# Optimization experiments

Hardware: AMD Instinct MI355X
Metric: run time of the kernel (lower is better)

Reference implementation:

```python
import jax, jax.numpy as jnp
import numpy as np

HEADS = 8
EMB = 128

def setup_inputs() -> dict:
    key = jax.random.key(0)
    ks = jax.random.split(key, 5)
    b, t, hin = 4, 128, 1024
    N = 50000
    x = jax.random.normal(ks[0], (b, t, hin), dtype=jnp.float32)
    curiosity_score = jax.random.normal(ks[1], (b, t), dtype=jnp.float32)
    Wq = jax.random.normal(ks[2], (EMB * HEADS, hin), dtype=jnp.float32) * (1.0 / np.sqrt(hin))
    keys = jax.random.normal(ks[3], (N, EMB), dtype=jnp.float32)
    values = jax.random.normal(ks[4], (N,), dtype=jnp.float32)
    return {"x": x, "curiosity_score": curiosity_score, "Wq": Wq, "keys": keys, "values": values}

def reference(x, curiosity_score, Wq, keys, values):
    b, t, hin = x.shape
    h, e = HEADS, EMB
    # query projection (torch Linear, no bias): x @ Wq.T -> (b, t, h*e)
    q = jnp.einsum('bti,oi->bto', x, Wq).reshape(b, t, h, e)
    q = q / (e ** 0.25)
    # scores vs shared offline key bank (N, e); buffer was `heads` identical copies,
    # so broadcasting over h is the same math without materializing repeats.
    scores = jnp.einsum('bthe,ne->bthn', q, keys)          # (b, t, h, N)
    attn = jax.nn.softmax(scores, axis=-1)
    # weighted sum of scalar values; curiosity adds a per-query constant to every
    # value, and since attn rows sum to 1 this equals adding curiosity afterwards.
    out = jnp.einsum('bthn,n->bth', attn, values) + curiosity_score[:, :, None]
    out = out.mean(axis=2)                                  # mean over heads
    return out[:, :, None]                                  # (b, t, 1)
```

## Files before the change

kernel.cpp:

```cpp
#include <hip/hip_runtime.h>

#define NHEADS   8
#define EMB_     128
#define BT_      512
#define HIN_     1024
#define NQ_      4096
#define NKEY_    50000
#define NPAD_    50048
#define TILES_TOT 782
#define TPS_     17
#define NSLICES_ 46

#define QSCALE   (0.29730177875068026f * 1.4426950408889634f)

typedef __attribute__((ext_vector_type(8))) short short8v;
typedef __attribute__((ext_vector_type(4))) float float4v;

#if __has_builtin(__builtin_amdgcn_exp2f)
#define EXP2F(x) __builtin_amdgcn_exp2f(x)
#else
#define EXP2F(x) exp2f(x)
#endif

__device__ __forceinline__ short f2bf(float f) {
  unsigned u = __float_as_uint(f);
  u += 0x7fffu + ((u >> 16) & 1u);
  return (short)(u >> 16);
}

#if __has_builtin(__builtin_amdgcn_cvt_pk_bf16_f32)
typedef __attribute__((ext_vector_type(2))) __bf16 bf16x2;
__device__ __forceinline__ unsigned pk2(float a, float b) {
  bf16x2 r = __builtin_amdgcn_cvt_pk_bf16_f32(a, b);
  union { bf16x2 v; unsigned u; } c; c.v = r; return c.u;
}
#else
__device__ __forceinline__ unsigned pk2(float a, float b) {
  return (unsigned)(unsigned short)f2bf(a) | ((unsigned)(unsigned short)f2bf(b) << 16);
}
#endif

__global__ __launch_bounds__(256) void convert_kernel(
    const float* __restrict__ keys, const float* __restrict__ values,
    short* __restrict__ keys_sw, float* __restrict__ vpad) {
#pragma unroll
  for (int j = 0; j < 2; ++j) {
    int g = blockIdx.x * 512 + j * 256 + threadIdx.x;
    int key  = g >> 5;
    int posf = g & 31;
    int lc   = posf >> 1;
    int half = posf & 1;
    union { short4 s; unsigned u[2]; } o;
    if (key < NKEY_) {
      float4 v = ((const float4*)keys)[g];
      o.u[0] = pk2(v.x, v.y);
      o.u[1] = pk2(v.z, v.w);
    } else {
      o.u[0] = 0; o.u[1] = 0;
    }
    int pc = lc ^ (key & 15);
    *(short4*)(keys_sw + key * 128 + pc * 8 + half * 4) = o.s;
    if (posf == 0) vpad[key] = (key < NKEY_) ? values[key] : 0.f;
  }
}

__global__ __launch_bounds__(256) void proj_kernel(
    const float* __restrict__ x, const float* __restrict__ Wq,
    short* __restrict__ qb) {
  const int wave = threadIdx.x >> 6, lane = threadIdx.x & 63;
  const int quad = lane >> 4, ln = lane & 15;
  const int tile = blockIdx.x * 4 + wave;
  const int mt = tile >> 6, ot = tile & 63;
  const float* xrow = x  + (mt * 16 + ln) * HIN_ + quad * 8;
  const float* wrow = Wq + (ot * 16 + ln) * HIN_ + quad * 8;
  float4v d = {0.f, 0.f, 0.f, 0.f};

  float4 xa0 = *(const float4*)(xrow);
  float4 xa1 = *(const float4*)(xrow + 4);
  float4 wa0 = *(const float4*)(wrow);
  float4 wa1 = *(const float4*)(wrow + 4);
  float4 xb0 = *(const float4*)(xrow + 32);
  float4 xb1 = *(const float4*)(xrow + 36);
  float4 wb0 = *(const float4*)(wrow + 32);
  float4 wb1 = *(const float4*)(wrow + 36);

#pragma unroll 1
  for (int k0 = 0; k0 < HIN_; k0 += 64) {
    union { short8v s8; unsigned u[4]; } af, bf;
    af.u[0] = pk2(xa0.x, xa0.y); af.u[1] = pk2(xa0.z, xa0.w);
    af.u[2] = pk2(xa1.x, xa1.y); af.u[3] = pk2(xa1.z, xa1.w);
    bf.u[0] = pk2(wa0.x, wa0.y); bf.u[1] = pk2(wa0.z, wa0.w);
    bf.u[2] = pk2(wa1.x, wa1.y); bf.u[3] = pk2(wa1.z, wa1.w);
    if (k0 + 64 < HIN_) {
      xa0 = *(const float4*)(xrow + k0 + 64);
      xa1 = *(const float4*)(xrow + k0 + 68);
      wa0 = *(const float4*)(wrow + k0 + 64);
      wa1 = *(const float4*)(wrow + k0 + 68);
    }
    d = __builtin_amdgcn_mfma_f32_16x16x32_bf16(af.s8, bf.s8, d, 0, 0, 0);

    af.u[0] = pk2(xb0.x, xb0.y); af.u[1] = pk2(xb0.z, xb0.w);
    af.u[2] = pk2(xb1.x, xb1.y); af.u[3] = pk2(xb1.z, xb1.w);
    bf.u[0] = pk2(wb0.x, wb0.y); bf.u[1] = pk2(wb0.z, wb0.w);
    bf.u[2] = pk2(wb1.x, wb1.y); bf.u[3] = pk2(wb1.z, wb1.w);
    if (k0 + 96 < HIN_) {
      xb0 = *(const float4*)(xrow + k0 + 96);
      xb1 = *(const float4*)(xrow + k0 + 100);
      wb0 = *(const float4*)(wrow + k0 + 96);
      wb1 = *(const float4*)(wrow + k0 + 100);
    }
    d = __builtin_amdgcn_mfma_f32_16x16x32_bf16(af.s8, bf.s8, d, 0, 0, 0);
  }
#pragma unroll
  for (int r2 = 0; r2 < 4; ++r2)
    qb[(mt * 16 + quad * 4 + r2) * HIN_ + ot * 16 + ln] = f2bf(d[r2] * QSCALE);
}

__global__ __launch_bounds__(256) void attn_kernel(
    const short* __restrict__ qb,
    const short* __restrict__ keys_sw,
    const float* __restrict__ vpad,
    float* __restrict__ partials) {
  __shared__ __align__(16) short kt[2][64 * 128];
  const int t     = threadIdx.x;
  const int wave  = t >> 6;
  const int lane  = t & 63;
  const int quad  = lane >> 4;
  const int ln    = lane & 15;
  const int qbase = blockIdx.x * 256 + wave * 64;
  const int slice = blockIdx.y;
  const int tile0 = slice * TPS_;
  const int tile1 = tile0 + TPS_;

  short8v a[4][4];
#pragma unroll
  for (int sub = 0; sub < 4; ++sub)
#pragma unroll
    for (int ks = 0; ks < 4; ++ks)
      a[sub][ks] = *(const short8v*)(qb + (qbase + sub * 16 + ln) * EMB_ + ks * 32 + quad * 8);

  float lsum[4][4], asum[4][4];
#pragma unroll
  for (int i = 0; i < 4; ++i)
#pragma unroll
    for (int j = 0; j < 4; ++j) { lsum[i][j] = 0.f; asum[i][j] = 0.f; }

  short8v stage[4];
  float vcur, vnext;
  {
    const short* src = keys_sw + tile0 * (64 * 128);
#pragma unroll
    for (int j = 0; j < 4; ++j)
      stage[j] = *(const short8v*)(src + (t + j * 256) * 8);
    vcur = vpad[tile0 * 64 + lane];
#pragma unroll
    for (int j = 0; j < 4; ++j)
      *(short8v*)(&kt[0][0] + (t + j * 256) * 8) = stage[j];
    const short* s1 = keys_sw + (tile0 + 1) * (64 * 128);
#pragma unroll
    for (int j = 0; j < 4; ++j)
      stage[j] = *(const short8v*)(s1 + (t + j * 256) * 8);
    vnext = vpad[(tile0 + 1) * 64 + lane];
  }
  __syncthreads();

  for (int tile = tile0; tile < tile1; ++tile) {
    const int cur = (tile - tile0) & 1;
    if (tile + 1 < tile1) {
#pragma unroll
      for (int j = 0; j < 4; ++j)
        *(short8v*)(&kt[cur ^ 1][0] + (t + j * 256) * 8) = stage[j];
    }
    const float vt = vcur;
    vcur = vnext;
    if (tile + 2 < tile1) {
      const short* nsrc = keys_sw + (tile + 2) * (64 * 128);
#pragma unroll
      for (int j = 0; j < 4; ++j)
        stage[j] = *(const short8v*)(nsrc + (t + j * 256) * 8);
      vnext = vpad[(tile + 2) * 64 + lane];
    }
#pragma unroll
    for (int nsub = 0; nsub < 4; ++nsub) {
      short8v b[4];
#pragma unroll
      for (int ks = 0; ks < 4; ++ks) {
        int kc = ks * 4 + quad;
        b[ks] = *(const short8v*)(&kt[cur][0] + (nsub * 16 + ln) * EMB_ + ((kc ^ ln) * 8));
      }
      float v = __shfl(vt, nsub * 16 + ln, 64);
      float4v d[4];
#pragma unroll
      for (int sub = 0; sub < 4; ++sub) d[sub] = (float4v){0.f, 0.f, 0.f, 0.f};
#pragma unroll
      for (int ks = 0; ks < 4; ++ks)
#pragma unroll
        for (int sub = 0; sub < 4; ++sub)
          d[sub] = __builtin_amdgcn_mfma_f32_16x16x32_bf16(a[sub][ks], b[ks], d[sub], 0, 0, 0);
#pragma unroll
      for (int sub = 0; sub < 4; ++sub)
#pragma unroll
        for (int r2 = 0; r2 < 4; ++r2) {
          float p = EXP2F(d[sub][r2]);
          lsum[sub][r2] += p;
          asum[sub][r2] = fmaf(p, v, asum[sub][r2]);
        }
    }
    __syncthreads();
  }

#pragma unroll
  for (int sub = 0; sub < 4; ++sub)
#pragma unroll
    for (int r2 = 0; r2 < 4; ++r2) {
      float L = lsum[sub][r2], A = asum[sub][r2];
#pragma unroll
      for (int m = 1; m < 16; m <<= 1) {
        L += __shfl_xor(L, m, 64);
        A += __shfl_xor(A, m, 64);
      }
      if (ln == 0) {
        int q = qbase + sub * 16 + quad * 4 + r2;
        partials[(q * NSLICES_ + slice) * 2 + 0] = L;
        partials[(q * NSLICES_ + slice) * 2 + 1] = A;
      }
    }
}

__global__ __launch_bounds__(256) void finalize_kernel(
    const float* __restrict__ partials, const float* __restrict__ cur,
    float* __restrict__ out) {
  int tid = blockIdx.x * 256 + threadIdx.x;
  int bt = tid >> 3, h = tid & 7;
  int q = bt * NHEADS + h;
  const float4* p = (const float4*)(partials + q * NSLICES_ * 2);
  float sl = 0.f, sa = 0.f;
#pragma unroll
  for (int i = 0; i < NSLICES_ / 2; ++i) {
    float4 v = p[i];
    sl += v.x + v.z;
    sa += v.y + v.w;
  }
  float r = sa / sl;
  r += __shfl_xor(r, 1, 64);
  r += __shfl_xor(r, 2, 64);
  r += __shfl_xor(r, 4, 64);
  if (h == 0) out[bt] = r * (1.f / NHEADS) + cur[bt];
}

extern "C" void kernel_launch(void* const* d_in, const int* in_sizes, int n_in,
                              void* d_out, int out_size, void* d_ws, size_t ws_size,
                              hipStream_t stream) {
  (void)in_sizes; (void)n_in; (void)out_size; (void)ws_size;
  const float* x      = (const float*)d_in[0];
  const float* cur    = (const float*)d_in[1];
  const float* Wq     = (const float*)d_in[2];
  const float* keys   = (const float*)d_in[3];
  const float* values = (const float*)d_in[4];
  float* out = (float*)d_out;

  char* ws = (char*)d_ws;
  short* keys_sw = (short*)(ws);
  float* vpad    = (float*)(ws + 12812288);
  short* qb      = (short*)(ws + 13012480);
  float* part    = (float*)(ws + 14061056);

  hipLaunchKernelGGL(convert_kernel, dim3((NPAD_ * 32) / 512), dim3(256), 0, stream,
                     keys, values, keys_sw, vpad);
  hipLaunchKernelGGL(proj_kernel, dim3(512), dim3(256), 0, stream, x, Wq, qb);
  hipLaunchKernelGGL(attn_kernel, dim3(16, NSLICES_), dim3(256), 0, stream,
                     qb, keys_sw, vpad, part);
  hipLaunchKernelGGL(finalize_kernel, dim3(16), dim3(256), 0, stream, part, cur, out);
}
```

Measured before the change: 176.3 us.

## Store keys in MFMA fragment order and load B operands directly from global

The convert kernel now writes the bf16 keys in the exact per-lane MFMA B-fragment order, in groups of 16 keys. The attention kernel then drops the shared-memory double buffer and its block barriers. Each wave loads its B fragments straight from global memory (L2/L1) with a two-group register prefetch. This removes LDS traffic and __syncthreads. The cost is that each of the four waves loads the same key data redundantly from cache, and the loads have less latency hiding than the block-staged tiles did.

```diff
diff --git a/kernel.cpp b/kernel.cpp
--- a/kernel.cpp
+++ b/kernel.cpp
@@ -7,8 +7,8 @@
 #define NQ_      4096
 #define NKEY_    50000
 #define NPAD_    50048
-#define TILES_TOT 782
-#define TPS_     17
+#define NGRP_    3128
+#define GPS_     68
 #define NSLICES_ 46
 
 #define QSCALE   (0.29730177875068026f * 1.4426950408889634f)
@@ -42,7 +42,7 @@
 
 __global__ __launch_bounds__(256) void convert_kernel(
     const float* __restrict__ keys, const float* __restrict__ values,
-    short* __restrict__ keys_sw, float* __restrict__ vpad) {
+    short* __restrict__ keys_fr, float* __restrict__ vpad) {
 #pragma unroll
   for (int j = 0; j < 2; ++j) {
     int g = blockIdx.x * 512 + j * 256 + threadIdx.x;
@@ -58,8 +58,9 @@
     } else {
       o.u[0] = 0; o.u[1] = 0;
     }
-    int pc = lc ^ (key & 15);
-    *(short4*)(keys_sw + key * 128 + pc * 8 + half * 4) = o.s;
+    int grp = key >> 4, kln = key & 15;
+    int ks = lc >> 2, q = lc & 3;
+    *(short4*)(keys_fr + ((grp * 4 + ks) * 64 + q * 16 + kln) * 8 + half * 4) = o.s;
     if (posf == 0) vpad[key] = (key < NKEY_) ? values[key] : 0.f;
   }
 }
@@ -118,10 +119,9 @@
 
 __global__ __launch_bounds__(256) void attn_kernel(
     const short* __restrict__ qb,
-    const short* __restrict__ keys_sw,
+    const short* __restrict__ keys_fr,
     const float* __restrict__ vpad,
     float* __restrict__ partials) {
-  __shared__ __align__(16) short kt[2][64 * 128];
   const int t     = threadIdx.x;
   const int wave  = t >> 6;
   const int lane  = t & 63;
@@ -129,8 +129,8 @@
   const int ln    = lane & 15;
   const int qbase = blockIdx.x * 256 + wave * 64;
   const int slice = blockIdx.y;
-  const int tile0 = slice * TPS_;
-  const int tile1 = tile0 + TPS_;
+  const int g0    = slice * GPS_;
+  const int g1    = g0 + GPS_;
 
   short8v a[4][4];
 #pragma unroll
@@ -145,50 +145,20 @@
 #pragma unroll
     for (int j = 0; j < 4; ++j) { lsum[i][j] = 0.f; asum[i][j] = 0.f; }
 
-  short8v stage[4];
-  float vcur, vnext;
-  {
-    const short* src = keys_sw + tile0 * (64 * 128);
-#pragma unroll
-    for (int j = 0; j < 4; ++j)
-      stage[j] = *(const short8v*)(src + (t + j * 256) * 8);
-    vcur = vpad[tile0 * 64 + lane];
-#pragma unroll
-    for (int j = 0; j < 4; ++j)
-      *(short8v*)(&kt[0][0] + (t + j * 256) * 8) = stage[j];
-    const short* s1 = keys_sw + (tile0 + 1) * (64 * 128);
-#pragma unroll
-    for (int j = 0; j < 4; ++j)
-      stage[j] = *(const short8v*)(s1 + (t + j * 256) * 8);
-    vnext = vpad[(tile0 + 1) * 64 + lane];
-  }
-  __syncthreads();
-
-  for (int tile = tile0; tile < tile1; ++tile) {
-    const int cur = (tile - tile0) & 1;
-    if (tile + 1 < tile1) {
-#pragma unroll
-      for (int j = 0; j < 4; ++j)
-        *(short8v*)(&kt[cur ^ 1][0] + (t + j * 256) * 8) = stage[j];
-    }
-    const float vt = vcur;
-    vcur = vnext;
-    if (tile + 2 < tile1) {
-      const short* nsrc = keys_sw + (tile + 2) * (64 * 128);
-#pragma unroll
-      for (int j = 0; j < 4; ++j)
-        stage[j] = *(const short8v*)(nsrc + (t + j * 256) * 8);
-      vnext = vpad[(tile + 2) * 64 + lane];
-    }
-#pragma unroll
-    for (int nsub = 0; nsub < 4; ++nsub) {
-      short8v b[4];
-#pragma unroll
-      for (int ks = 0; ks < 4; ++ks) {
-        int kc = ks * 4 + quad;
-        b[ks] = *(const short8v*)(&kt[cur][0] + (nsub * 16 + ln) * EMB_ + ((kc ^ ln) * 8));
-      }
-      float v = __shfl(vt, nsub * 16 + ln, 64);
+  short8v bA[4], bB[4];
+  float vA, vB;
+#pragma unroll
+  for (int ks = 0; ks < 4; ++ks)
+    bA[ks] = *(const short8v*)(keys_fr + ((g0 * 4 + ks) * 64 + lane) * 8);
+  vA = vpad[g0 * 16 + ln];
+#pragma unroll
+  for (int ks = 0; ks < 4; ++ks)
+    bB[ks] = *(const short8v*)(keys_fr + (((g0 + 1) * 4 + ks) * 64 + lane) * 8);
+  vB = vpad[(g0 + 1) * 16 + ln];
+
+#pragma unroll 1
+  for (int g = g0; g < g1; g += 2) {
+    {
       float4v d[4];
 #pragma unroll
       for (int sub = 0; sub < 4; ++sub) d[sub] = (float4v){0.f, 0.f, 0.f, 0.f};
@@ -196,17 +166,48 @@
       for (int ks = 0; ks < 4; ++ks)
 #pragma unroll
         for (int sub = 0; sub < 4; ++sub)
-          d[sub] = __builtin_amdgcn_mfma_f32_16x16x32_bf16(a[sub][ks], b[ks], d[sub], 0, 0, 0);
+          d[sub] = __builtin_amdgcn_mfma_f32_16x16x32_bf16(a[sub][ks], bA[ks], d[sub], 0, 0, 0);
+      if (g + 2 < g1) {
+#pragma unroll
+        for (int ks = 0; ks < 4; ++ks)
+          bA[ks] = *(const short8v*)(keys_fr + (((g + 2) * 4 + ks) * 64 + lane) * 8);
+      }
+      float vv = vA;
+      if (g + 2 < g1) vA = vpad[(g + 2) * 16 + ln];
 #pragma unroll
       for (int sub = 0; sub < 4; ++sub)
 #pragma unroll
         for (int r2 = 0; r2 < 4; ++r2) {
           float p = EXP2F(d[sub][r2]);
           lsum[sub][r2] += p;
-          asum[sub][r2] = fmaf(p, v, asum[sub][r2]);
+          asum[sub][r2] = fmaf(p, vv, asum[sub][r2]);
         }
     }
-    __syncthreads();
+    {
+      float4v d[4];
+#pragma unroll
+      for (int sub = 0; sub < 4; ++sub) d[sub] = (float4v){0.f, 0.f, 0.f, 0.f};
+#pragma unroll
+      for (int ks = 0; ks < 4; ++ks)
+#pragma unroll
+        for (int sub = 0; sub < 4; ++sub)
+          d[sub] = __builtin_amdgcn_mfma_f32_16x16x32_bf16(a[sub][ks], bB[ks], d[sub], 0, 0, 0);
+      if (g + 3 < g1) {
+#pragma unroll
+        for (int ks = 0; ks < 4; ++ks)
+          bB[ks] = *(const short8v*)(keys_fr + (((g + 3) * 4 + ks) * 64 + lane) * 8);
+      }
+      float vv = vB;
+      if (g + 3 < g1) vB = vpad[(g + 3) * 16 + ln];
+#pragma unroll
+      for (int sub = 0; sub < 4; ++sub)
+#pragma unroll
+        for (int r2 = 0; r2 < 4; ++r2) {
+          float p = EXP2F(d[sub][r2]);
+          lsum[sub][r2] += p;
+          asum[sub][r2] = fmaf(p, vv, asum[sub][r2]);
+        }
+    }
   }
 
 #pragma unroll
@@ -260,15 +261,15 @@
   float* out = (float*)d_out;
 
   char* ws = (char*)d_ws;
-  short* keys_sw = (short*)(ws);
+  short* keys_fr = (short*)(ws);
   float* vpad    = (float*)(ws + 12812288);
   short* qb      = (short*)(ws + 13012480);
   float* part    = (float*)(ws + 14061056);
 
   hipLaunchKernelGGL(convert_kernel, dim3((NPAD_ * 32) / 512), dim3(256), 0, stream,
-                     keys, values, keys_sw, vpad);
+                     keys, values, keys_fr, vpad);
   hipLaunchKernelGGL(proj_kernel, dim3(512), dim3(256), 0, stream, x, Wq, qb);
   hipLaunchKernelGGL(attn_kernel, dim3(16, NSLICES_), dim3(256), 0, stream,
-                     qb, keys_sw, vpad, part);
+                     qb, keys_fr, vpad, part);
   hipLaunchKernelGGL(finalize_kernel, dim3(16), dim3(256), 0, stream, part, cur, out);
 }
```

Result: no change. 175.2 us (median of 2 runs) (-0.6%).
